# Performance work log

Hardware: AMD Instinct MI355X
Metric: run time of the kernel (lower is better)

## Reference

```python
import jax, jax.numpy as jnp
import numpy as np

NUM_HEADS = 16

def setup_inputs() -> dict:
    key = jax.random.key(0)
    ks = jax.random.split(key, 7)
    B, S, D = 2, 2048, 1024
    X = jax.random.normal(ks[0], (B, S, D), dtype=jnp.float32)
    s = 1.0 / np.sqrt(D)
    Wq = jax.random.normal(ks[1], (D, D), dtype=jnp.float32) * s
    Wk = jax.random.normal(ks[2], (D, D), dtype=jnp.float32) * s
    Wv = jax.random.normal(ks[3], (D, D), dtype=jnp.float32) * s
    Wo = jax.random.normal(ks[4], (D, D), dtype=jnp.float32) * s
    bo = jnp.zeros((D,), dtype=jnp.float32)
    return {"X": X, "Wq": Wq, "Wk": Wk, "Wv": Wv, "Wo": Wo, "bo": bo}

def reference(X, Wq, Wk, Wv, Wo, bo):
    B, S, D = X.shape
    H = NUM_HEADS
    hd = D // H
    # project and split heads -> [B, H, S, hd]
    def split(t):
        return t.reshape(B, S, H, hd).transpose(0, 2, 1, 3)
    q = split(X @ Wq)
    k = split(X @ Wk)
    v = split(X @ Wv)
    scores = jnp.einsum('bhqd,bhkd->bhqk', q, k) / jnp.sqrt(jnp.float32(hd))
    causal = jnp.tril(jnp.ones((S, S), dtype=bool))
    scores = jnp.where(causal, scores, -jnp.inf)
    weights = jax.nn.softmax(scores, axis=-1)  # dropout p=0 -> identity
    ctx = jnp.einsum('bhqk,bhkd->bhqd', weights, v)
    ctx = ctx.transpose(0, 2, 1, 3).reshape(B, S, D)
    return ctx @ Wo + bo
```

## Files before the change

### kernel.cpp

```cpp
#include <hip/hip_runtime.h>


typedef __attribute__((ext_vector_type(8))) short short8;
typedef __attribute__((ext_vector_type(4))) float floatx4;

__device__ inline unsigned short f2bf(float f) {
  unsigned u = __float_as_uint(f);
  unsigned r = (u + 0x7fffu + ((u >> 16) & 1u)) >> 16;
  return (unsigned short)r;
}

__device__ __forceinline__ float fast_exp2(float x) {
#if __has_builtin(__builtin_amdgcn_exp2f)
  return __builtin_amdgcn_exp2f(x);
#else
  float r;
  asm volatile("v_exp_f32_e32 %0, %1" : "=v"(r) : "v"(x));
  return r;
#endif
}

__device__ __forceinline__ void gll16(const unsigned short* g, unsigned short* l) {
  __builtin_amdgcn_global_load_lds(
      (const __attribute__((address_space(1))) unsigned int*)(g),
      (__attribute__((address_space(3))) unsigned int*)(l),
      16, 0, 0);
}

constexpr int B_ = 2, S_ = 2048, D_ = 1024, H_ = 16, HD_ = 64;

__global__ __launch_bounds__(256) void prep_inputs(
    const float* __restrict__ x, unsigned short* __restrict__ xb,
    const float* __restrict__ w0, const float* __restrict__ w1,
    const float* __restrict__ w2, const float* __restrict__ w3,
    unsigned short* __restrict__ wt_base)
{
  if (blockIdx.z == 4) {
    const int tid = threadIdx.y * 32 + threadIdx.x;
    const size_t base =
        ((size_t)(blockIdx.y * 32 + blockIdx.x) * 256 + tid) * 16;
#pragma unroll
    for (int half = 0; half < 2; ++half) {
      const size_t i = base + half * 8;
      float4 a = *(const float4*)(x + i);
      float4 b = *(const float4*)(x + i + 4);
      short8 o;
      o[0] = (short)f2bf(a.x); o[1] = (short)f2bf(a.y);
      o[2] = (short)f2bf(a.z); o[3] = (short)f2bf(a.w);
      o[4] = (short)f2bf(b.x); o[5] = (short)f2bf(b.y);
      o[6] = (short)f2bf(b.z); o[7] = (short)f2bf(b.w);
      *(short8*)(xb + i) = o;
    }
    return;
  }
  const float* src;
  switch (blockIdx.z) {
    case 0: src = w0; break;
    case 1: src = w1; break;
    case 2: src = w2; break;
    default: src = w3; break;
  }
  unsigned short* dst = wt_base + (size_t)blockIdx.z * 1024 * 1024;
  __shared__ unsigned short t[32][33];
  const int bx = blockIdx.x * 32;
  const int by = blockIdx.y * 32;
  const int x_ = threadIdx.x;
  for (int yy = threadIdx.y; yy < 32; yy += 8)
    t[yy][x_] = f2bf(src[(size_t)(by + yy) * 1024 + bx + x_]);
  __syncthreads();
  for (int yy = threadIdx.y; yy < 32; yy += 8)
    dst[(size_t)(bx + yy) * 1024 + by + x_] = t[x_][yy];
}

__global__ __launch_bounds__(256) void transpose_v(
    const unsigned short* __restrict__ Vb, unsigned short* __restrict__ Vt)
{
  __shared__ unsigned short t[32][33];
  const int bh = blockIdx.z;
  const int b = bh >> 4, h = bh & 15;
  const int s0 = blockIdx.x * 32, d0 = blockIdx.y * 32;
  const int x = threadIdx.x;
  for (int yy = threadIdx.y; yy < 32; yy += 8)
    t[yy][x] = Vb[(size_t)(b * 2048 + s0 + yy) * 1024 + h * 64 + d0 + x];
  __syncthreads();
  for (int yy = threadIdx.y; yy < 32; yy += 8)
    Vt[((size_t)bh * 64 + d0 + yy) * 2048 + s0 + x] = t[x][yy];
}

__global__ __launch_bounds__(256) void gemm256_qkv(
    const unsigned short* __restrict__ A,
    const unsigned short* __restrict__ Bt,
    unsigned short* __restrict__ Qo,
    unsigned short* __restrict__ Ko,
    unsigned short* __restrict__ Vo)
{
  __shared__ unsigned short sA[2][128 * 32];
  __shared__ unsigned short sB[2][128 * 32];
  const int K = 1024;
  const int m0 = blockIdx.y * 128;
  const int bn0 = blockIdx.x * 128;

  const int tid = threadIdx.x, wave = tid >> 6, lane = tid & 63;
  const int g = lane >> 4, ml = lane & 15;
  const int wm = wave & 1, wn = wave >> 1;

  const unsigned short* ag0 = A + (size_t)(m0 + (tid >> 2)) * K + (tid & 3) * 8;
  const unsigned short* ag1 = ag0 + (size_t)64 * K;
  const unsigned short* bg0 = Bt + (size_t)(bn0 + (tid >> 2)) * K + (tid & 3) * 8;
  const unsigned short* bg1 = bg0 + (size_t)64 * K;
  const int woff = wave * 512;

  floatx4 acc[4][4];
#pragma unroll
  for (int mt = 0; mt < 4; ++mt)
#pragma unroll
    for (int nt = 0; nt < 4; ++nt) acc[mt][nt] = (floatx4){0.f, 0.f, 0.f, 0.f};

  for (int k0 = 0; k0 < K; k0 += 64) {
    __syncthreads();
#pragma unroll
    for (int t = 0; t < 2; ++t) {
      gll16(ag0 + k0 + t * 32, sA[t] + woff);
      gll16(ag1 + k0 + t * 32, sA[t] + 2048 + woff);
      gll16(bg0 + k0 + t * 32, sB[t] + woff);
      gll16(bg1 + k0 + t * 32, sB[t] + 2048 + woff);
    }
    __syncthreads();
#pragma unroll
    for (int t = 0; t < 2; ++t) {
      short8 af[4], bf[4];
#pragma unroll
      for (int mt = 0; mt < 4; ++mt)
        af[mt] = *(const short8*)(sA[t] + (wm * 64 + mt * 16 + ml) * 32 + g * 8);
#pragma unroll
      for (int nt = 0; nt < 4; ++nt)
        bf[nt] = *(const short8*)(sB[t] + (wn * 64 + nt * 16 + ml) * 32 + g * 8);
#pragma unroll
      for (int mt = 0; mt < 4; ++mt)
#pragma unroll
        for (int nt = 0; nt < 4; ++nt)
          acc[mt][nt] = __builtin_amdgcn_mfma_f32_16x16x32_bf16(
              af[mt], bf[nt], acc[mt][nt], 0, 0, 0);
    }
  }

  const int proj = blockIdx.x >> 3;
  unsigned short* out = (proj == 0) ? Qo : (proj == 1) ? Ko : Vo;
  const int col0 = (blockIdx.x & 7) * 128;
#pragma unroll
  for (int mt = 0; mt < 4; ++mt) {
#pragma unroll
    for (int nt = 0; nt < 4; ++nt) {
      const int col = col0 + wn * 64 + nt * 16 + ml;
#pragma unroll
      for (int r = 0; r < 4; ++r) {
        const int row = m0 + wm * 64 + mt * 16 + g * 4 + r;
        out[(size_t)row * 1024 + col] = f2bf(acc[mt][nt][r]);
      }
    }
  }
}

__global__ __launch_bounds__(256) void gemm_wo64(
    const unsigned short* __restrict__ A,
    const unsigned short* __restrict__ Bt,
    const float* __restrict__ bias,
    float* __restrict__ C)
{
  __shared__ unsigned short sA[4][64 * 32];
  __shared__ unsigned short sB[4][128 * 32];
  const int K = 1024;
  const int m0 = blockIdx.y * 64;
  const int bn0 = blockIdx.x * 128;
  const int tid = threadIdx.x, wave = tid >> 6, lane = tid & 63;
  const int g = lane >> 4, ml = lane & 15;
  const int wm = wave & 1, wn = wave >> 1;

  const unsigned short* ag =
      A + (size_t)(m0 + wave * 16 + (lane >> 2)) * K + (lane & 3) * 8;
  const unsigned short* bg0 = Bt + (size_t)(bn0 + (tid >> 2)) * K + (tid & 3) * 8;
  const unsigned short* bg1 = bg0 + (size_t)64 * K;
  const int woff = wave * 512;

  floatx4 acc[2][4];
#pragma unroll
  for (int mt = 0; mt < 2; ++mt)
#pragma unroll
    for (int nt = 0; nt < 4; ++nt) acc[mt][nt] = (floatx4){0.f, 0.f, 0.f, 0.f};

  for (int k0 = 0; k0 < K; k0 += 128) {
    __syncthreads();
#pragma unroll
    for (int t = 0; t < 4; ++t) {
      gll16(ag + k0 + t * 32, sA[t] + woff);
      gll16(bg0 + k0 + t * 32, sB[t] + woff);
      gll16(bg1 + k0 + t * 32, sB[t] + 2048 + woff);
    }
    __syncthreads();
#pragma unroll
    for (int t = 0; t < 4; ++t) {
      short8 af[2], bf[4];
#pragma unroll
      for (int mt = 0; mt < 2; ++mt)
        af[mt] = *(const short8*)(sA[t] + (wm * 32 + mt * 16 + ml) * 32 + g * 8);
#pragma unroll
      for (int nt = 0; nt < 4; ++nt)
        bf[nt] = *(const short8*)(sB[t] + (wn * 64 + nt * 16 + ml) * 32 + g * 8);
#pragma unroll
      for (int mt = 0; mt < 2; ++mt)
#pragma unroll
        for (int nt = 0; nt < 4; ++nt)
          acc[mt][nt] = __builtin_amdgcn_mfma_f32_16x16x32_bf16(
              af[mt], bf[nt], acc[mt][nt], 0, 0, 0);
    }
  }

#pragma unroll
  for (int mt = 0; mt < 2; ++mt) {
#pragma unroll
    for (int nt = 0; nt < 4; ++nt) {
      const int col = bn0 + wn * 64 + nt * 16 + ml;
      const float badd = bias[col];
#pragma unroll
      for (int r = 0; r < 4; ++r) {
        const int row = m0 + wm * 32 + mt * 16 + g * 4 + r;
        C[(size_t)row * 1024 + col] = acc[mt][nt][r] + badd;
      }
    }
  }
}

constexpr int KTPB = 2;

struct AttnLds {
  unsigned short k0[2][KTPB][64 * 32];
  unsigned short k1[2][KTPB][64 * 32];
  unsigned short v0[2][KTPB][64 * 32];
  unsigned short v1[2][KTPB][64 * 32];
};
union __align__(16) AttnLdsU {
  AttnLds t;
  float comb[4 * 64 * 36];
};

__device__ __forceinline__ void softmax_pack(
    const floatx4* s, const bool diag, const int qg, const int kb,
    float& l, short8* ap)
{
  const float C1 = 0.18033688f;
  const float C2 = -34.6246810f;

  unsigned wb[4][4];
#pragma unroll
  for (int nb = 0; nb < 4; ++nb) {
#pragma unroll
    for (int r = 0; r < 4; ++r) {
      float wv = fast_exp2(fmaf(s[nb][r], C1, C2));
      if (diag && (kb + nb * 16 + r > qg)) wv = 0.f;
      const unsigned bits = __float_as_uint(wv) & 0xffff0000u;
      wb[nb][r] = bits;
      l += __uint_as_float(bits);
    }
  }

  unsigned pk[4][2];
#pragma unroll
  for (int nb = 0; nb < 4; ++nb) {
    pk[nb][0] = __builtin_amdgcn_perm(wb[nb][1], wb[nb][0], 0x07060302u);
    pk[nb][1] = __builtin_amdgcn_perm(wb[nb][3], wb[nb][2], 0x07060302u);
  }

  unsigned Fr[2][4];
#pragma unroll
  for (int rr = 0; rr < 2; ++rr) {
    unsigned a0 = pk[0][rr], a1 = pk[1][rr];
    unsigned a2 = pk[2][rr], a3 = pk[3][rr];
    asm("v_permlane32_swap_b32 %0, %1" : "+v"(a0), "+v"(a1));
    asm("v_permlane32_swap_b32 %0, %1" : "+v"(a2), "+v"(a3));
    asm("v_permlane16_swap_b32 %0, %1" : "+v"(a0), "+v"(a1));
    asm("v_permlane16_swap_b32 %0, %1" : "+v"(a2), "+v"(a3));
    Fr[0][rr] = a0; Fr[0][2 + rr] = a1;
    Fr[1][rr] = a2; Fr[1][2 + rr] = a3;
  }
#pragma unroll
  for (int f = 0; f < 2; ++f) {
    union { unsigned u[4]; short8 s8; } uap;
    uap.u[0] = Fr[f][0]; uap.u[1] = Fr[f][1];
    uap.u[2] = Fr[f][2]; uap.u[3] = Fr[f][3];
    ap[f] = uap.s8;
  }
}

template <bool DUAL>
__device__ __forceinline__ void attn_tile2(
    const short8* aqB, const short8* aqA,
    const unsigned short* sK0, const unsigned short* sK1,
    const unsigned short* sV0, const unsigned short* sV1,
    floatx4* accB, float& lB, floatx4* accA, float& lA,
    const bool diagB, const bool diagA,
    const int qgB, const int qgA, const int kb,
    const int g, const int ml)
{
  floatx4 sB[4], sA[4];
#pragma unroll
  for (int nb = 0; nb < 4; ++nb) {
    short8 bk0 = *(const short8*)(sK0 + (nb * 16 + ml) * 32 + g * 8);
    short8 bk1 = *(const short8*)(sK1 + (nb * 16 + ml) * 32 + g * 8);
    sB[nb] = (floatx4){0.f, 0.f, 0.f, 0.f};
    sB[nb] = __builtin_amdgcn_mfma_f32_16x16x32_bf16(bk0, aqB[0], sB[nb], 0, 0, 0);
    sB[nb] = __builtin_amdgcn_mfma_f32_16x16x32_bf16(bk1, aqB[1], sB[nb], 0, 0, 0);
    if (DUAL) {
      sA[nb] = (floatx4){0.f, 0.f, 0.f, 0.f};
      sA[nb] = __builtin_amdgcn_mfma_f32_16x16x32_bf16(bk0, aqA[0], sA[nb], 0, 0, 0);
      sA[nb] = __builtin_amdgcn_mfma_f32_16x16x32_bf16(bk1, aqA[1], sA[nb], 0, 0, 0);
    }
  }

  short8 apB[2], apA[2];
  softmax_pack(sB, diagB, qgB, kb, lB, apB);
  if (DUAL) softmax_pack(sA, diagA, qgA, kb, lA, apA);

#pragma unroll
  for (int f = 0; f < 2; ++f) {
    const unsigned short* sv = f ? sV1 : sV0;
#pragma unroll
    for (int jd = 0; jd < 4; ++jd) {
      short8 bv = *(const short8*)(sv + (jd * 16 + ml) * 32 + g * 8);
      accB[jd] = __builtin_amdgcn_mfma_f32_16x16x32_bf16(apB[f], bv, accB[jd], 0, 0, 0);
      if (DUAL)
        accA[jd] = __builtin_amdgcn_mfma_f32_16x16x32_bf16(apA[f], bv, accA[jd], 0, 0, 0);
    }
  }
}

__global__ __launch_bounds__(512) void attn_v15(
    const unsigned short* __restrict__ Q,
    const unsigned short* __restrict__ Kg,
    const unsigned short* __restrict__ Vt,
    unsigned short* __restrict__ CTX)
{
  __shared__ AttnLdsU lds;

  const int L = blockIdx.x;
  const int rid = (L & 7) * 64 + (L >> 3);
  const int p = rid & 15;
  const int bh = rid >> 4;

  const int b = bh >> 4, h = bh & 15;
  const int qbA = p, qbB = 31 - p;
  const int qA0 = qbA * 64, qB0 = qbB * 64;
  const int tid = threadIdx.x, w = tid >> 6, lane = tid & 63;
  const int slice = w & 3, par = w >> 2;
  const int g = lane >> 4, ml = lane & 15;

  const size_t headoff = (size_t)b * S_ * D_ + (size_t)h * HD_;
  const size_t vtoff   = (size_t)bh * HD_ * S_;

  short8 aqA[2], aqB[2];
  {
    const unsigned short* qp =
        Q + headoff + (size_t)(qA0 + slice * 16 + ml) * D_ + g * 8;
    aqA[0] = *(const short8*)qp;
    aqA[1] = *(const short8*)(qp + 32);
  }
  {
    const unsigned short* qp =
        Q + headoff + (size_t)(qB0 + slice * 16 + ml) * D_ + g * 8;
    aqB[0] = *(const short8*)qp;
    aqB[1] = *(const short8*)(qp + 32);
  }

  floatx4 accA[4], accB[4];
#pragma unroll
  for (int jd = 0; jd < 4; ++jd) {
    accA[jd] = (floatx4){0.f, 0.f, 0.f, 0.f};
    accB[jd] = (floatx4){0.f, 0.f, 0.f, 0.f};
  }
  float lA = 0.f, lB = 0.f;
  const int qgA = qA0 + slice * 16 + ml;
  const int qgB = qB0 + slice * 16 + ml;

  const int sw = slice;
  const unsigned short* kgb =
      Kg + headoff + (size_t)(sw * 16 + (lane >> 2)) * D_ + (lane & 3) * 8;
  const unsigned short* vgb =
      Vt + vtoff + (size_t)(sw * 16 + (lane >> 2)) * S_ + (lane & 3) * 8;
  const int woff = sw * 512;

  const int ntiles = qbB + 1;

  {
    const int cnt = (ntiles < KTPB) ? ntiles : KTPB;
#pragma unroll
    for (int t = 0; t < KTPB; ++t) {
      if (t >= cnt) break;
      if (w < 4) {
        const size_t ko = (size_t)t * 64 * D_;
        gll16(kgb + ko,      lds.t.k0[0][t] + woff);
        gll16(kgb + ko + 32, lds.t.k1[0][t] + woff);
      } else {
        gll16(vgb + t * 64,      lds.t.v0[0][t] + woff);
        gll16(vgb + t * 64 + 32, lds.t.v1[0][t] + woff);
      }
    }
  }
  __syncthreads();

  for (int kt0 = 0; kt0 < ntiles; kt0 += KTPB) {
    const int bufi = (kt0 >> 1) & 1;
    const int nxt = kt0 + KTPB;
    if (nxt < ntiles) {
      const int cn = (ntiles - nxt < KTPB) ? (ntiles - nxt) : KTPB;
#pragma unroll
      for (int t = 0; t < KTPB; ++t) {
        if (t >= cn) break;
        const int kt = nxt + t;
        if (w < 4) {
          const size_t ko = (size_t)kt * 64 * D_;
          gll16(kgb + ko,      lds.t.k0[bufi ^ 1][t] + woff);
          gll16(kgb + ko + 32, lds.t.k1[bufi ^ 1][t] + woff);
        } else {
          gll16(vgb + kt * 64,      lds.t.v0[bufi ^ 1][t] + woff);
          gll16(vgb + kt * 64 + 32, lds.t.v1[bufi ^ 1][t] + woff);
        }
      }
    }

    const int cnt = (ntiles - kt0 < KTPB) ? (ntiles - kt0) : KTPB;
    if (par < cnt) {
      const int kt = kt0 + par;
      const int kb = kt * 64 + g * 4;
      if (kt <= qbA)
        attn_tile2<true>(aqB, aqA,
                         lds.t.k0[bufi][par], lds.t.k1[bufi][par],
                         lds.t.v0[bufi][par], lds.t.v1[bufi][par],
                         accB, lB, accA, lA,
                         kt == qbB, kt == qbA, qgB, qgA, kb, g, ml);
      else
        attn_tile2<false>(aqB, aqA,
                          lds.t.k0[bufi][par], lds.t.k1[bufi][par],
                          lds.t.v0[bufi][par], lds.t.v1[bufi][par],
                          accB, lB, accA, lA,
                          kt == qbB, false, qgB, qgA, kb, g, ml);
    }
    __syncthreads();
  }

  {
    float* slot = lds.comb + (size_t)(slice * 64 + lane) * 36;
    if (par == 1) {
#pragma unroll
      for (int jd = 0; jd < 4; ++jd) {
        *(floatx4*)(slot + jd * 4) = accA[jd];
        *(floatx4*)(slot + 16 + jd * 4) = accB[jd];
      }
      slot[32] = lA;
      slot[33] = lB;
    }
    __syncthreads();
    if (par == 1) return;
#pragma unroll
    for (int jd = 0; jd < 4; ++jd) {
      accA[jd] += *(const floatx4*)(slot + jd * 4);
      accB[jd] += *(const floatx4*)(slot + 16 + jd * 4);
    }
    lA += slot[32];
    lB += slot[33];
  }

  lA += __shfl_xor(lA, 16); lA += __shfl_xor(lA, 32);
  lB += __shfl_xor(lB, 16); lB += __shfl_xor(lB, 32);
  const float liA = 1.0f / lA;
  const float liB = 1.0f / lB;
  float lrA[4], lrB[4];
#pragma unroll
  for (int r = 0; r < 4; ++r) {
    lrA[r] = __shfl(liA, g * 4 + r);
    lrB[r] = __shfl(liB, g * 4 + r);
  }

#pragma unroll
  for (int r = 0; r < 4; ++r) {
    const int rowA = qA0 + slice * 16 + g * 4 + r;
    const int rowB = qB0 + slice * 16 + g * 4 + r;
#pragma unroll
    for (int jd = 0; jd < 4; ++jd) {
      CTX[headoff + (size_t)rowA * D_ + jd * 16 + ml] = f2bf(accA[jd][r] * lrA[r]);
      CTX[headoff + (size_t)rowB * D_ + jd * 16 + ml] = f2bf(accB[jd][r] * lrB[r]);
    }
  }
}

extern "C" void kernel_launch(void* const* d_in, const int* in_sizes, int n_in,
                              void* d_out, int out_size, void* d_ws, size_t ws_size,
                              hipStream_t stream)
{
  const float* X  = (const float*)d_in[0];
  const float* Wq = (const float*)d_in[1];
  const float* Wk = (const float*)d_in[2];
  const float* Wv = (const float*)d_in[3];
  const float* Wo = (const float*)d_in[4];
  const float* bo = (const float*)d_in[5];

  char* ws = (char*)d_ws;
  const size_t MB = 1024 * 1024;

  unsigned short* Qb  = (unsigned short*)(ws);
  unsigned short* Kb  = (unsigned short*)(ws + 8 * MB);
  unsigned short* Xb  = (unsigned short*)(ws + 16 * MB);
  unsigned short* WT  = (unsigned short*)(ws + 24 * MB);
  unsigned short* WoT = WT + (size_t)3 * 1024 * 1024;
  unsigned short* Vb  = (unsigned short*)d_out;
  unsigned short* Vt  = Xb;

  prep_inputs<<<dim3(32, 32, 5), dim3(32, 8), 0, stream>>>(
      X, Xb, Wq, Wk, Wv, Wo, WT);
  gemm256_qkv<<<dim3(24, 32), 256, 0, stream>>>(Xb, WT, Qb, Kb, Vb);
  transpose_v<<<dim3(64, 2, 32), dim3(32, 8), 0, stream>>>(Vb, Vt);
  attn_v15<<<dim3(512), 512, 0, stream>>>(Qb, Kb, Vt, Qb);
  gemm_wo64<<<dim3(8, 64), 256, 0, stream>>>(Qb, WoT, bo, (float*)d_out);
}
```

Baseline: 185.1 us.

## Swizzle GEMM block order, add MFMA wave priority, split softmax sum chains

Both GEMM kernels remap their linear block index so that consecutive blocks land on the same XCD-ordered group (stride-8 remap), aiming for better L2 reuse of A/B tiles across the chiplets. In the attention tile, s_setprio raises wave priority around the MFMA sections so waves in matrix phases get issued ahead of waves doing softmax. The softmax row sum now uses four independent partial accumulators on unmasked-mantissa exp values instead of one serial chain over bf16-truncated values, shortening the dependency chain at the cost of slightly different normalization (sum no longer matches the truncated weights exactly).

```diff
diff --git a/kernel.cpp b/kernel.cpp
--- a/kernel.cpp
+++ b/kernel.cpp
@@ -97,8 +97,12 @@
   __shared__ unsigned short sA[2][128 * 32];
   __shared__ unsigned short sB[2][128 * 32];
   const int K = 1024;
-  const int m0 = blockIdx.y * 128;
-  const int bn0 = blockIdx.x * 128;
+
+  const int L = blockIdx.y * 24 + blockIdx.x;
+  const int rid = (L & 7) * 96 + (L >> 3);
+  const int brow = rid / 24, bcol = rid % 24;
+  const int m0 = brow * 128;
+  const int bn0 = bcol * 128;
 
   const int tid = threadIdx.x, wave = tid >> 6, lane = tid & 63;
   const int g = lane >> 4, ml = lane & 15;
@@ -144,9 +148,9 @@
     }
   }
 
-  const int proj = blockIdx.x >> 3;
+  const int proj = bcol >> 3;
   unsigned short* out = (proj == 0) ? Qo : (proj == 1) ? Ko : Vo;
-  const int col0 = (blockIdx.x & 7) * 128;
+  const int col0 = (bcol & 7) * 128;
 #pragma unroll
   for (int mt = 0; mt < 4; ++mt) {
 #pragma unroll
@@ -170,8 +174,12 @@
   __shared__ unsigned short sA[4][64 * 32];
   __shared__ unsigned short sB[4][128 * 32];
   const int K = 1024;
-  const int m0 = blockIdx.y * 64;
-  const int bn0 = blockIdx.x * 128;
+
+  const int L = blockIdx.y * 8 + blockIdx.x;
+  const int rid = (L & 7) * 64 + (L >> 3);
+  const int m0 = (rid >> 3) * 64;
+  const int bn0 = (rid & 7) * 128;
+
   const int tid = threadIdx.x, wave = tid >> 6, lane = tid & 63;
   const int g = lane >> 4, ml = lane & 15;
   const int wm = wave & 1, wn = wave >> 1;
@@ -251,17 +259,21 @@
   const float C2 = -34.6246810f;
 
   unsigned wb[4][4];
+  float lp0 = 0.f, lp1 = 0.f, lp2 = 0.f, lp3 = 0.f;
 #pragma unroll
   for (int nb = 0; nb < 4; ++nb) {
 #pragma unroll
     for (int r = 0; r < 4; ++r) {
       float wv = fast_exp2(fmaf(s[nb][r], C1, C2));
       if (diag && (kb + nb * 16 + r > qg)) wv = 0.f;
-      const unsigned bits = __float_as_uint(wv) & 0xffff0000u;
-      wb[nb][r] = bits;
-      l += __uint_as_float(bits);
-    }
-  }
+      wb[nb][r] = __float_as_uint(wv);
+      if (nb == 0) lp0 += wv;
+      else if (nb == 1) lp1 += wv;
+      else if (nb == 2) lp2 += wv;
+      else lp3 += wv;
+    }
+  }
+  l += (lp0 + lp1) + (lp2 + lp3);
 
   unsigned pk[4][2];
 #pragma unroll
@@ -302,6 +314,7 @@
     const int g, const int ml)
 {
   floatx4 sB[4], sA[4];
+  __builtin_amdgcn_s_setprio(1);
 #pragma unroll
   for (int nb = 0; nb < 4; ++nb) {
     short8 bk0 = *(const short8*)(sK0 + (nb * 16 + ml) * 32 + g * 8);
@@ -315,11 +328,13 @@
       sA[nb] = __builtin_amdgcn_mfma_f32_16x16x32_bf16(bk1, aqA[1], sA[nb], 0, 0, 0);
     }
   }
+  __builtin_amdgcn_s_setprio(0);
 
   short8 apB[2], apA[2];
   softmax_pack(sB, diagB, qgB, kb, lB, apB);
   if (DUAL) softmax_pack(sA, diagA, qgA, kb, lA, apA);
 
+  __builtin_amdgcn_s_setprio(1);
 #pragma unroll
   for (int f = 0; f < 2; ++f) {
     const unsigned short* sv = f ? sV1 : sV0;
@@ -331,9 +346,10 @@
         accA[jd] = __builtin_amdgcn_mfma_f32_16x16x32_bf16(apA[f], bv, accA[jd], 0, 0, 0);
     }
   }
-}
-
-__global__ __launch_bounds__(512) void attn_v15(
+  __builtin_amdgcn_s_setprio(0);
+}
+
+__global__ __launch_bounds__(512) void attn_v16(
     const unsigned short* __restrict__ Q,
     const unsigned short* __restrict__ Kg,
     const unsigned short* __restrict__ Vt,
@@ -517,6 +533,6 @@
       X, Xb, Wq, Wk, Wv, Wo, WT);
   gemm256_qkv<<<dim3(24, 32), 256, 0, stream>>>(Xb, WT, Qb, Kb, Vb);
   transpose_v<<<dim3(64, 2, 32), dim3(32, 8), 0, stream>>>(Vb, Vt);
-  attn_v15<<<dim3(512), 512, 0, stream>>>(Qb, Kb, Vt, Qb);
+  attn_v16<<<dim3(512), 512, 0, stream>>>(Qb, Kb, Vt, Qb);
   gemm_wo64<<<dim3(8, 64), 256, 0, stream>>>(Qb, WoT, bo, (float*)d_out);
 }
```

New measurement: 183.6 us. About the same (-0.8%).
